# Performance work log

Measured on AMD Instinct MI355X. Metric: run time of the kernel, lower is better.

The kernel has to match this reference:

```python
import jax, jax.numpy as jnp
import numpy as np

B, S, D, H = 1, 4096, 768, 12
HD = D // H  # 64

def setup_inputs() -> dict:
    key = jax.random.key(0)
    k1, k2, k3 = jax.random.split(key, 3)
    x = jax.random.normal(k1, (B, S, D), dtype=jnp.float32)
    W_attn = jax.random.normal(k2, (D, 3 * D), dtype=jnp.float32) * 0.02
    b_attn = jnp.zeros((3 * D,), dtype=jnp.float32)
    W_proj = jax.random.normal(k3, (D, D), dtype=jnp.float32) * 0.02
    b_proj = jnp.zeros((D,), dtype=jnp.float32)
    return {"x": x, "W_attn": W_attn, "b_attn": b_attn, "W_proj": W_proj, "b_proj": b_proj}

def reference(x, W_attn, b_attn, W_proj, b_proj):
    # qkv projection (Conv1D = x @ W + b)
    qkv = x @ W_attn + b_attn  # [B,S,3D]
    q, k, v = jnp.split(qkv, 3, axis=-1)
    def split_heads(t):
        return t.reshape(B, S, H, HD).transpose(0, 2, 1, 3)  # [B,H,S,HD]
    q, k, v = split_heads(q), split_heads(k), split_heads(v)
    # NOTE: original applies no 1/sqrt(head_dim) scaling
    scores = jnp.einsum('bhqd,bhkd->bhqk', q, k)  # [B,H,S,S]
    causal = jnp.tril(jnp.ones((S, S), dtype=bool))
    mask_value = jnp.finfo(scores.dtype).min
    scores = jnp.where(causal, scores, mask_value)
    attn = jax.nn.softmax(scores, axis=-1)
    # dropout is identity in eval mode
    out = jnp.einsum('bhqk,bhkd->bhqd', attn, v)  # [B,H,S,HD]
    out = out.transpose(0, 2, 1, 3).reshape(B, S, D)
    return out @ W_proj + b_proj
```

## Files before the change

### kernel.cpp

```cpp
#include <hip/hip_runtime.h>


typedef short bf16x8 __attribute__((ext_vector_type(8)));
typedef float f32x4 __attribute__((ext_vector_type(4)));
typedef unsigned short u16x8_t __attribute__((ext_vector_type(8)));
typedef unsigned short u16x4_t __attribute__((ext_vector_type(4)));

#define ATT_S  4096
#define ATT_D  768
#define ATT_3D 2304
#define ATT_H  12
#define LOG2E  1.44269504089f

__device__ __forceinline__ unsigned short f2b(float f) {
  union { float f; unsigned int u; } v; v.f = f;
  unsigned int r = v.u + 0x7fffu + ((v.u >> 16) & 1u);
  return (unsigned short)(r >> 16);
}
__device__ __forceinline__ float b2f(unsigned short b) {
  union { unsigned int u; float f; } v; v.u = ((unsigned int)b) << 16;
  return v.f;
}

__device__ __forceinline__ f32x4 mfma16(bf16x8 a, bf16x8 b, f32x4 c) {
  return __builtin_amdgcn_mfma_f32_16x16x32_bf16(a, b, c, 0, 0, 0);
}

__device__ __forceinline__ void glds16(const void* g, void* l) {
  __builtin_amdgcn_global_load_lds((__attribute__((address_space(1))) void*)g,
                                   (__attribute__((address_space(3))) void*)l,
                                   16, 0, 0);
}

__device__ __forceinline__ int swz8(int row, int c) {
  return row * 64 + ((c ^ (row & 7)) << 3);
}


__global__ __launch_bounds__(256) void convert_f32_bf16(
    const float* __restrict__ in, unsigned short* __restrict__ out, int n4) {
  int i = blockIdx.x * 256 + threadIdx.x;
  if (i >= n4) return;
  float4 v = ((const float4*)in)[i];
  u16x4_t o;
  o[0] = f2b(v.x); o[1] = f2b(v.y); o[2] = f2b(v.z); o[3] = f2b(v.w);
  ((u16x4_t*)out)[i] = o;
}

__global__ __launch_bounds__(256) void transpose_conv(
    const float* __restrict__ W, unsigned short* __restrict__ WT, int K, int N) {
  __shared__ float tile[32][33];
  int bx = blockIdx.x, by = blockIdx.y;
  int tx = threadIdx.x & 31, ty = threadIdx.x >> 5;
#pragma unroll
  for (int k = 0; k < 4; k++)
    tile[ty + k * 8][tx] = W[(size_t)(by * 32 + ty + k * 8) * N + bx * 32 + tx];
  __syncthreads();
#pragma unroll
  for (int k = 0; k < 4; k++)
    WT[(size_t)(bx * 32 + ty + k * 8) * K + by * 32 + tx] = f2b(tile[tx][ty + k * 8]);
}


template <int BF16_OUT>
__global__ __launch_bounds__(256) void gemm_bias(
    const unsigned short* __restrict__ A, const unsigned short* __restrict__ Bt,
    const float* __restrict__ bias, void* __restrict__ Cout,
    int M, int N, int K) {
  __shared__ unsigned short As[128 * 32];
  __shared__ unsigned short Bs[128 * 32];
  const int t = threadIdx.x;
  const int lane = t & 63;
  const int wave = t >> 6;
  const int wr = wave >> 1, wc = wave & 1;
  const int rl = lane & 15, rg = lane >> 4;

  const int nbn = N >> 7;
  const int nwg = gridDim.x;
  const int bid = blockIdx.x;
  const int cpx = nwg >> 3;
  const int swz = (bid & 7) * cpx + (bid >> 3);
  const int bm = swz / nbn, bn = swz % nbn;

  const unsigned short* Ab = A + (size_t)bm * 128 * K;
  const unsigned short* Bb = Bt + (size_t)bn * 128 * K;

  f32x4 acc[4][4];
#pragma unroll
  for (int m = 0; m < 4; m++)
#pragma unroll
    for (int n = 0; n < 4; n++) acc[m][n] = (f32x4){0.f, 0.f, 0.f, 0.f};

  for (int kt = 0; kt < K; kt += 32) {
    if (kt) __syncthreads();
#pragma unroll
    for (int it = 0; it < 2; ++it) {
      int idx = it * 256 + t;
      int row = idx >> 2;
      int slot = idx & 3;
      int sl2 = slot ^ ((row >> 1) & 3);
      unsigned short* ldsA = As + (size_t)(it * 256 + wave * 64) * 8;
      unsigned short* ldsB = Bs + (size_t)(it * 256 + wave * 64) * 8;
      glds16(Ab + (size_t)row * K + kt + sl2 * 8, ldsA);
      glds16(Bb + (size_t)row * K + kt + sl2 * 8, ldsB);
    }
    __syncthreads();

    bf16x8 a[4], b[4];
#pragma unroll
    for (int m = 0; m < 4; m++) {
      int row = wr * 64 + m * 16 + rl;
      int sl2 = rg ^ ((row >> 1) & 3);
      a[m] = *(const bf16x8*)&As[row * 32 + sl2 * 8];
    }
#pragma unroll
    for (int n = 0; n < 4; n++) {
      int row = wc * 64 + n * 16 + rl;
      int sl2 = rg ^ ((row >> 1) & 3);
      b[n] = *(const bf16x8*)&Bs[row * 32 + sl2 * 8];
    }
#pragma unroll
    for (int m = 0; m < 4; m++)
#pragma unroll
      for (int n = 0; n < 4; n++)
        acc[m][n] = mfma16(a[m], b[n], acc[m][n]);
  }

#pragma unroll
  for (int n = 0; n < 4; n++) {
    int col = bn * 128 + wc * 64 + n * 16 + rl;
    float bv = bias[col];
#pragma unroll
    for (int m = 0; m < 4; m++) {
      int row0 = bm * 128 + wr * 64 + m * 16 + rg * 4;
#pragma unroll
      for (int i = 0; i < 4; i++) {
        float v = acc[m][n][i] + bv;
        if (BF16_OUT)
          ((unsigned short*)Cout)[(size_t)(row0 + i) * N + col] = f2b(v);
        else
          ((float*)Cout)[(size_t)(row0 + i) * N + col] = v;
      }
    }
  }
}


__global__ __launch_bounds__(256) void attn_fwd(
    const unsigned short* __restrict__ qkv, unsigned short* __restrict__ aout,
    unsigned short* __restrict__ pscr, float* __restrict__ ml) {
  __shared__ unsigned short Kb[2][64 * 64];
  __shared__ unsigned short Vb[2][64 * 64];
  __shared__ unsigned short Ps[4][16 * 64];

  const int tid = threadIdx.x;
  const int lane = tid & 63;
  const int w = tid >> 6;
  const int rl = lane & 15, rg = lane >> 4;

  const int bid = blockIdx.x;
  const int h = bid % ATT_H;
  const int u = 159 - (bid / ATT_H);
  int qb, ck;
  if (u < 16)      { qb = u;                 ck = 0; }
  else if (u < 48) { qb = 16 + ((u - 16) >> 1); ck = (u - 16) & 1; }
  else if (u < 96) { qb = 32 + (u - 48) / 3;    ck = (u - 48) % 3; }
  else             { qb = 48 + ((u - 96) >> 2); ck = (u - 96) & 3; }

  const int nt = qb + 1;
  const int t0 = ck * 16;
  const int t1 = min(nt, t0 + 16);
  const int qbase = qb * 64 + w * 16;

  unsigned short* Pw = Ps[w];
  const int skey = lane >> 3;
  const int slot = lane & 7;

  bf16x8 qf[2];
#pragma unroll
  for (int ks = 0; ks < 2; ks++)
    qf[ks] = *(const bf16x8*)&qkv[(size_t)(qbase + rl) * ATT_3D + h * 64 + ks * 32 + rg * 8];

  float mS = -3.0e38f, lS = 0.f;
  f32x4 oacc[4];
#pragma unroll
  for (int hf = 0; hf < 4; hf++) oacc[hf] = (f32x4){0.f, 0.f, 0.f, 0.f};

  u16x8_t kr[2], vr[2];
  const size_t gstep = (size_t)64 * ATT_3D;
  size_t gbase = (size_t)(w * 8 + skey) * ATT_3D + 768 + h * 64 + slot * 8;

#pragma unroll
  for (int it = 0; it < 2; ++it) {
    kr[it] = *(const u16x8_t*)&qkv[gbase + (size_t)t0 * gstep + it * 32 * ATT_3D];
    vr[it] = *(const u16x8_t*)&qkv[gbase + (size_t)t0 * gstep + it * 32 * ATT_3D + 768];
  }
  {
#pragma unroll
    for (int it = 0; it < 2; ++it) {
      int key = it * 32 + w * 8 + skey;
      *(u16x8_t*)&Kb[0][swz8(key, slot)] = kr[it];
      *(u16x8_t*)&Pw[swz8(it * 8 + skey, slot)] = vr[it];
    }
#pragma unroll
    for (int kk = 0; kk < 2; ++kk) {
      u16x8_t g;
#pragma unroll
      for (int j = 0; j < 8; j++)
        g[j] = Pw[swz8(kk * 8 + j, lane >> 3) + (lane & 7)];
      *(u16x8_t*)&Vb[0][swz8(lane, kk * 4 + w)] = g;
    }
  }
  __syncthreads();

  for (int t = t0; t < t1; ++t) {
    const int cur = t & 1;
    const bool pref = (t + 1 < t1);
    if (pref) {
      size_t gb = gbase + (size_t)(t + 1) * gstep;
#pragma unroll
      for (int it = 0; it < 2; ++it) {
        kr[it] = *(const u16x8_t*)&qkv[gb + it * 32 * ATT_3D];
        vr[it] = *(const u16x8_t*)&qkv[gb + it * 32 * ATT_3D + 768];
      }
    }

    f32x4 st[4];
#pragma unroll
    for (int kf = 0; kf < 4; kf++) st[kf] = (f32x4){0.f, 0.f, 0.f, 0.f};
    __builtin_amdgcn_s_setprio(1);
#pragma unroll
    for (int ks = 0; ks < 2; ks++) {
#pragma unroll
      for (int kf = 0; kf < 4; kf++) {
        bf16x8 kfr = *(const bf16x8*)&Kb[cur][swz8(kf * 16 + rl, ks * 4 + rg)];
        st[kf] = mfma16(kfr, qf[ks], st[kf]);
      }
    }
    __builtin_amdgcn_s_setprio(0);

    if (t == nt - 1) {
#pragma unroll
      for (int kf = 0; kf < 4; kf++)
#pragma unroll
        for (int i = 0; i < 4; i++) {
          int key = t * 64 + kf * 16 + rg * 4 + i;
          if (key > qbase + rl) st[kf][i] = -3.0e38f;
        }
    }

    float pm = st[0][0];
#pragma unroll
    for (int kf = 0; kf < 4; kf++)
#pragma unroll
      for (int i = 0; i < 4; i++) pm = fmaxf(pm, st[kf][i]);
    pm = fmaxf(pm, __shfl_xor(pm, 16, 64));
    pm = fmaxf(pm, __shfl_xor(pm, 32, 64));
    if (!__all(pm - mS <= 8.f)) {
      float mn = fmaxf(mS, pm);
      float fac = __expf(mS - mn);
      mS = mn;
      lS *= fac;
#pragma unroll
      for (int i = 0; i < 4; i++) {
        float fi = __shfl(fac, rg * 4 + i, 64);
#pragma unroll
        for (int hf = 0; hf < 4; hf++) oacc[hf][i] *= fi;
      }
    }
    const float mC = mS * LOG2E;
    float psum = 0.f;
#pragma unroll
    for (int kf = 0; kf < 4; kf++) {
      u16x4_t pw4;
#pragma unroll
      for (int i = 0; i < 4; i++) {
        float p = __builtin_amdgcn_exp2f(fmaf(st[kf][i], LOG2E, -mC));
        psum += p;
        pw4[i] = f2b(p);
      }
      *(u16x4_t*)&Pw[swz8(rl, kf * 2 + (rg >> 1)) + (rg & 1) * 4] = pw4;
    }
    psum += __shfl_xor(psum, 16, 64);
    psum += __shfl_xor(psum, 32, 64);
    lS += psum;

    __builtin_amdgcn_s_setprio(1);
#pragma unroll
    for (int ks2 = 0; ks2 < 2; ks2++) {
      bf16x8 pa = *(const bf16x8*)&Pw[swz8(rl, ks2 * 4 + rg)];
#pragma unroll
      for (int hf = 0; hf < 4; hf++) {
        bf16x8 vbf = *(const bf16x8*)&Vb[cur][swz8(hf * 16 + rl, ks2 * 4 + rg)];
        oacc[hf] = mfma16(pa, vbf, oacc[hf]);
      }
    }
    __builtin_amdgcn_s_setprio(0);

    if (pref) {
      const int nxt = cur ^ 1;
#pragma unroll
      for (int it = 0; it < 2; ++it) {
        int key = it * 32 + w * 8 + skey;
        *(u16x8_t*)&Kb[nxt][swz8(key, slot)] = kr[it];
        *(u16x8_t*)&Pw[swz8(it * 8 + skey, slot)] = vr[it];
      }
#pragma unroll
      for (int kk = 0; kk < 2; ++kk) {
        u16x8_t g;
#pragma unroll
        for (int j = 0; j < 8; j++)
          g[j] = Pw[swz8(kk * 8 + j, lane >> 3) + (lane & 7)];
        *(u16x8_t*)&Vb[nxt][swz8(lane, kk * 4 + w)] = g;
      }
    }
    __syncthreads();
  }

  const bool split = (qb >= 16);
  unsigned short* dst;
  int pitch;
  if (!split || ck == 0) {
    dst = aout + (size_t)(qb * 64) * ATT_D + h * 64;
    pitch = ATT_D;
  } else {
    int s;
    if (qb < 32)      s = h * 96 + (qb - 16);
    else if (qb < 48) s = h * 96 + 16 + (qb - 32) * 2 + (ck - 1);
    else              s = h * 96 + 48 + (qb - 48) * 3 + (ck - 1);
    dst = pscr + (size_t)s * 4096;
    pitch = 64;
  }
  if (split && rg == 0) {
    int unit = h * 48 + (qb - 16);
    float2* mlp = (float2*)ml;
    mlp[(unit * 4 + ck) * 64 + w * 16 + rl] = make_float2(mS, lS);
  }
#pragma unroll
  for (int i = 0; i < 4; i++) {
    float li = __shfl(lS, rg * 4 + i, 64);
    float inv = 1.f / li;
    int qrow = w * 16 + rg * 4 + i;
#pragma unroll
    for (int hf = 0; hf < 4; hf++)
      dst[(size_t)qrow * pitch + hf * 16 + rl] = f2b(oacc[hf][i] * inv);
  }
}


__global__ __launch_bounds__(256) void attn_combine(
    const unsigned short* __restrict__ pscr, const float* __restrict__ ml,
    unsigned short* __restrict__ ao) {
  const int unit = blockIdx.x;
  const int h = unit / 48, uqb = unit % 48, qb = uqb + 16;
  const int nch = (qb + 16) >> 4;
  const int tid = threadIdx.x;
  const int q = tid >> 2, part = tid & 3;

  const float2* mlp = (const float2*)ml;
  float m[4], l[4];
  float M = -3.0e38f;
  for (int c = 0; c < nch; ++c) {
    float2 p = mlp[(unit * 4 + c) * 64 + q];
    m[c] = p.x; l[c] = p.y;
    M = fmaxf(M, m[c]);
  }
  float wgt[4], den = 0.f;
  for (int c = 0; c < nch; ++c) {
    wgt[c] = l[c] * __expf(m[c] - M);
    den += wgt[c];
  }

  float acc[16];
#pragma unroll
  for (int j = 0; j < 16; j++) acc[j] = 0.f;

  unsigned short* aorow = ao + (size_t)(qb * 64 + q) * ATT_D + h * 64 + part * 16;
  for (int c = 0; c < nch; ++c) {
    const unsigned short* src;
    if (c == 0) {
      src = aorow;
    } else {
      int s;
      if (qb < 32)      s = h * 96 + (qb - 16);
      else if (qb < 48) s = h * 96 + 16 + (qb - 32) * 2 + (c - 1);
      else              s = h * 96 + 48 + (qb - 48) * 3 + (c - 1);
      src = pscr + (size_t)s * 4096 + q * 64 + part * 16;
    }
    u16x8_t v0 = *(const u16x8_t*)src;
    u16x8_t v1 = *(const u16x8_t*)(src + 8);
#pragma unroll
    for (int j = 0; j < 8; j++) acc[j] += wgt[c] * b2f(v0[j]);
#pragma unroll
    for (int j = 0; j < 8; j++) acc[8 + j] += wgt[c] * b2f(v1[j]);
  }
  float inv = 1.f / den;
  u16x8_t o0, o1;
#pragma unroll
  for (int j = 0; j < 8; j++) { o0[j] = f2b(acc[j] * inv); o1[j] = f2b(acc[8 + j] * inv); }
  *(u16x8_t*)aorow = o0;
  *(u16x8_t*)(aorow + 8) = o1;
}


extern "C" void kernel_launch(void* const* d_in, const int* in_sizes, int n_in,
                              void* d_out, int out_size, void* d_ws, size_t ws_size,
                              hipStream_t stream) {
  const float* x      = (const float*)d_in[0];
  const float* W_attn = (const float*)d_in[1];
  const float* b_attn = (const float*)d_in[2];
  const float* W_proj = (const float*)d_in[3];
  const float* b_proj = (const float*)d_in[4];
  float* out = (float*)d_out;

  char* ws = (char*)d_ws;
  unsigned short* xb  = (unsigned short*)(ws);
  unsigned short* WaT = (unsigned short*)(ws + 6291456);
  unsigned short* WpT = (unsigned short*)(ws + 9830400);
  unsigned short* qkv = (unsigned short*)(ws + 11010048);
  unsigned short* ao  = (unsigned short*)(ws + 29884416);
  unsigned short* pscr = (unsigned short*)(ws);
  float*          ml   = (float*)(ws + 9830400);

  convert_f32_bf16<<<3072, 256, 0, stream>>>(x, xb, 786432);
  transpose_conv<<<dim3(72, 24), 256, 0, stream>>>(W_attn, WaT, 768, 2304);

  gemm_bias<1><<<576, 256, 0, stream>>>(xb, WaT, b_attn, qkv, 4096, 2304, 768);
  attn_fwd<<<1920, 256, 0, stream>>>(qkv, ao, pscr, ml);
  attn_combine<<<576, 256, 0, stream>>>(pscr, ml, ao);

  transpose_conv<<<dim3(24, 24), 256, 0, stream>>>(W_proj, WpT, 768, 768);
  gemm_bias<0><<<192, 256, 0, stream>>>(ao, WpT, b_proj, out, 4096, 768, 768);
}
```

Baseline: 129.1 us.

## Single-buffer K/V tiles in LDS and raise occupancy hint to six blocks

Replaces the double-buffered K and V shared-memory tiles with single buffers, which halves their LDS footprint, and adds a minimum of six blocks per multiprocessor to the launch bounds. To make single buffering safe, the loop now has two barriers per iteration: K is refilled after the QK^T MFMAs and V after the PV MFMAs. The max reduction is also regrouped into a tree. More resident blocks can hide latency, but the extra barrier per tile adds synchronization stalls, and the occupancy hint may push the compiler to spill registers.

```diff
diff --git a/kernel.cpp b/kernel.cpp
--- a/kernel.cpp
+++ b/kernel.cpp
@@ -146,11 +146,11 @@
 }
 
 
-__global__ __launch_bounds__(256) void attn_fwd(
+__global__ __launch_bounds__(256, 6) void attn_fwd(
     const unsigned short* __restrict__ qkv, unsigned short* __restrict__ aout,
     unsigned short* __restrict__ pscr, float* __restrict__ ml) {
-  __shared__ unsigned short Kb[2][64 * 64];
-  __shared__ unsigned short Vb[2][64 * 64];
+  __shared__ unsigned short Kb[64 * 64];
+  __shared__ unsigned short Vb[64 * 64];
   __shared__ unsigned short Ps[4][16 * 64];
 
   const int tid = threadIdx.x;
@@ -199,7 +199,7 @@
 #pragma unroll
     for (int it = 0; it < 2; ++it) {
       int key = it * 32 + w * 8 + skey;
-      *(u16x8_t*)&Kb[0][swz8(key, slot)] = kr[it];
+      *(u16x8_t*)&Kb[swz8(key, slot)] = kr[it];
       *(u16x8_t*)&Pw[swz8(it * 8 + skey, slot)] = vr[it];
     }
 #pragma unroll
@@ -208,13 +208,12 @@
 #pragma unroll
       for (int j = 0; j < 8; j++)
         g[j] = Pw[swz8(kk * 8 + j, lane >> 3) + (lane & 7)];
-      *(u16x8_t*)&Vb[0][swz8(lane, kk * 4 + w)] = g;
+      *(u16x8_t*)&Vb[swz8(lane, kk * 4 + w)] = g;
     }
   }
   __syncthreads();
 
   for (int t = t0; t < t1; ++t) {
-    const int cur = t & 1;
     const bool pref = (t + 1 < t1);
     if (pref) {
       size_t gb = gbase + (size_t)(t + 1) * gstep;
@@ -233,11 +232,18 @@
     for (int ks = 0; ks < 2; ks++) {
 #pragma unroll
       for (int kf = 0; kf < 4; kf++) {
-        bf16x8 kfr = *(const bf16x8*)&Kb[cur][swz8(kf * 16 + rl, ks * 4 + rg)];
+        bf16x8 kfr = *(const bf16x8*)&Kb[swz8(kf * 16 + rl, ks * 4 + rg)];
         st[kf] = mfma16(kfr, qf[ks], st[kf]);
       }
     }
     __builtin_amdgcn_s_setprio(0);
+
+    __syncthreads();
+    if (pref) {
+#pragma unroll
+      for (int it = 0; it < 2; ++it)
+        *(u16x8_t*)&Kb[swz8(it * 32 + w * 8 + skey, slot)] = kr[it];
+    }
 
     if (t == nt - 1) {
 #pragma unroll
@@ -249,11 +255,11 @@
         }
     }
 
-    float pm = st[0][0];
-#pragma unroll
-    for (int kf = 0; kf < 4; kf++)
-#pragma unroll
-      for (int i = 0; i < 4; i++) pm = fmaxf(pm, st[kf][i]);
+    float pm = fmaxf(fmaxf(st[0][0], st[0][1]), fmaxf(st[0][2], st[0][3]));
+#pragma unroll
+    for (int kf = 1; kf < 4; kf++)
+      pm = fmaxf(pm, fmaxf(fmaxf(st[kf][0], st[kf][1]),
+                           fmaxf(st[kf][2], st[kf][3])));
     pm = fmaxf(pm, __shfl_xor(pm, 16, 64));
     pm = fmaxf(pm, __shfl_xor(pm, 32, 64));
     if (!__all(pm - mS <= 8.f)) {
@@ -291,30 +297,26 @@
       bf16x8 pa = *(const bf16x8*)&Pw[swz8(rl, ks2 * 4 + rg)];
 #pragma unroll
       for (int hf = 0; hf < 4; hf++) {
-        bf16x8 vbf = *(const bf16x8*)&Vb[cur][swz8(hf * 16 + rl, ks2 * 4 + rg)];
+        bf16x8 vbf = *(const bf16x8*)&Vb[swz8(hf * 16 + rl, ks2 * 4 + rg)];
         oacc[hf] = mfma16(pa, vbf, oacc[hf]);
       }
     }
     __builtin_amdgcn_s_setprio(0);
 
+    __syncthreads();
     if (pref) {
-      const int nxt = cur ^ 1;
-#pragma unroll
-      for (int it = 0; it < 2; ++it) {
-        int key = it * 32 + w * 8 + skey;
-        *(u16x8_t*)&Kb[nxt][swz8(key, slot)] = kr[it];
+#pragma unroll
+      for (int it = 0; it < 2; ++it)
         *(u16x8_t*)&Pw[swz8(it * 8 + skey, slot)] = vr[it];
-      }
 #pragma unroll
       for (int kk = 0; kk < 2; ++kk) {
         u16x8_t g;
 #pragma unroll
         for (int j = 0; j < 8; j++)
           g[j] = Pw[swz8(kk * 8 + j, lane >> 3) + (lane & 7)];
-        *(u16x8_t*)&Vb[nxt][swz8(lane, kk * 4 + w)] = g;
-      }
-    }
-    __syncthreads();
+        *(u16x8_t*)&Vb[swz8(lane, kk * 4 + w)] = g;
+      }
+    }
   }
 
   const bool split = (qb >= 16);
```

After: 190.7 us. 47.7% more time.
